# Kernel tuning notes

Hardware: AMD Instinct MI355X
Metric: run time of the kernel (lower is better)

Reference implementation:

```python
import math
import jax, jax.numpy as jnp
import numpy as np

N_HEADS = 16
D_EMBED = 1024
D_HEAD = D_EMBED // N_HEADS
B, S = 4, 2048


def setup_inputs() -> dict:
    key = jax.random.key(0)
    k1, k2, k3, k4, k5 = jax.random.split(key, 5)
    scale_in = 1.0 / math.sqrt(D_EMBED)
    return {
        "x": jax.random.normal(k1, (B, S, D_EMBED), dtype=jnp.float32),
        "w_in": jax.random.normal(k2, (3 * D_EMBED, D_EMBED), dtype=jnp.float32) * scale_in,
        "b_in": jax.random.normal(k3, (3 * D_EMBED,), dtype=jnp.float32) * 0.02,
        "w_out": jax.random.normal(k4, (D_EMBED, D_EMBED), dtype=jnp.float32) * scale_in,
        "b_out": jax.random.normal(k5, (D_EMBED,), dtype=jnp.float32) * 0.02,
        "causal_mask": 1,
    }


def reference(x, w_in, b_in, w_out, b_out, causal_mask):
    Bn, Sn, D = x.shape
    # fused QKV projection (torch Linear: x @ W.T + b)
    qkv = x @ w_in.T + b_in                       # (B, S, 3D)
    q, k, v = jnp.split(qkv, 3, axis=-1)
    def to_heads(t):
        return t.reshape(Bn, Sn, N_HEADS, D_HEAD).transpose(0, 2, 1, 3)  # (B,H,S,dh)
    q, k, v = to_heads(q), to_heads(k), to_heads(v)
    # manual scaled dot-product attention, full (B,H,S,S) scores
    scores = jnp.einsum("bhqd,bhkd->bhqk", q, k)
    if causal_mask:
        tri = jnp.triu(jnp.ones((Sn, Sn), dtype=bool), k=1)
        scores = jnp.where(tri, -jnp.inf, scores)
    scores = scores / math.sqrt(D_HEAD)
    weights = jax.nn.softmax(scores, axis=-1)
    out = jnp.einsum("bhqk,bhkd->bhqd", weights, v)  # (B,H,S,dh)
    out = out.transpose(0, 2, 1, 3).reshape(Bn, Sn, D)
    return out @ w_out.T + b_out
```

## Files before the change

### kernel.cpp

```cpp
#include <hip/hip_runtime.h>

typedef __bf16 bf16x8 __attribute__((ext_vector_type(8)));
typedef float  f32x4  __attribute__((ext_vector_type(4)));
typedef unsigned int uint;

__device__ inline unsigned short f2bf(float f) {
  union { float f; unsigned int u; } v; v.f = f;
  unsigned int u = v.u;
  unsigned int r = u + 0x7FFF + ((u >> 16) & 1);
  return (unsigned short)(r >> 16);
}

__device__ inline uint pack_bf16_rhu(float a, float b) {
  uint ua = __builtin_bit_cast(uint, a) + 0x8000u;
  uint ub = __builtin_bit_cast(uint, b) + 0x8000u;
  return __builtin_amdgcn_perm(ub, ua, 0x07060302u);
}

__device__ inline void load_lds16(const unsigned short* g, unsigned short* l) {
  __builtin_amdgcn_global_load_lds(
      (const __attribute__((address_space(1))) uint*)(g),
      (__attribute__((address_space(3))) uint*)(l), 16, 0, 0);
}

__device__ inline void cvt4(const float* in, unsigned short* out) {
  float4 f = *reinterpret_cast<const float4*>(in);
  ushort4 o;
  o.x = f2bf(f.x); o.y = f2bf(f.y); o.z = f2bf(f.z); o.w = f2bf(f.w);
  *reinterpret_cast<ushort4*>(out) = o;
}

__global__ void cvt_all(const float* __restrict__ x, const float* __restrict__ w_in,
                        const float* __restrict__ w_out,
                        unsigned short* __restrict__ x_bf,
                        unsigned short* __restrict__ w_in_bf,
                        unsigned short* __restrict__ w_out_bf) {
  const int n1 = 8192 * 1024, n2 = 3072 * 1024;
  int i = (blockIdx.x * blockDim.x + threadIdx.x) * 4;
  if (i < n1)            cvt4(x + i, x_bf + i);
  else if (i < n1 + n2)  cvt4(w_in + (i - n1), w_in_bf + (i - n1));
  else                   cvt4(w_out + (i - n1 - n2), w_out_bf + (i - n1 - n2));
}

template<bool OUT_BF16, bool VSPLIT>
__global__ __launch_bounds__(256) void gemm_bt128(
    const unsigned short* __restrict__ A,
    const unsigned short* __restrict__ B,
    const float* __restrict__ bias,
    void* __restrict__ Cout,
    unsigned short* __restrict__ vt,
    int M, int N, int K, int ldc, float scale, int ncut)
{
  __shared__ __attribute__((aligned(16))) unsigned short As[128 * 64];
  __shared__ __attribute__((aligned(16))) unsigned short Bs[128 * 64];

  const int t    = threadIdx.x;
  const int wave = t >> 6, lane = t & 63;
  const int l16  = lane & 15, quad = lane >> 4;
  const int wr = wave >> 1, wc = wave & 1;
  const int m0 = blockIdx.y * 128, n0 = blockIdx.x * 128;
  const int l8 = l16 & 7;

  f32x4 acc[4][4] = {};

  for (int k0 = 0; k0 < K; k0 += 64) {
#pragma unroll
    for (int i = 0; i < 4; ++i) {
      int chunk = i * 256 + t;
      int row = chunk >> 3, cb = chunk & 7;
      int gcb = cb ^ (row & 7);
      load_lds16(A + (size_t)(m0 + row) * K + k0 + gcb * 8, As + chunk * 8);
    }
#pragma unroll
    for (int i = 0; i < 4; ++i) {
      int chunk = i * 256 + t;
      int row = chunk >> 3, cb = chunk & 7;
      int gcb = cb ^ (row & 7);
      load_lds16(B + (size_t)(n0 + row) * K + k0 + gcb * 8, Bs + chunk * 8);
    }
    __syncthreads();
#pragma unroll
    for (int ks = 0; ks < 2; ++ks) {
      bf16x8 af[4], bfr[4];
#pragma unroll
      for (int mt = 0; mt < 4; ++mt)
        af[mt] = *(const bf16x8*)(As + (wr * 64 + mt * 16 + l16) * 64 +
                                  (((ks * 4 + quad) ^ l8) << 3));
#pragma unroll
      for (int nt = 0; nt < 4; ++nt)
        bfr[nt] = *(const bf16x8*)(Bs + (wc * 64 + nt * 16 + l16) * 64 +
                                   (((ks * 4 + quad) ^ l8) << 3));
#pragma unroll
      for (int mt = 0; mt < 4; ++mt)
#pragma unroll
        for (int nt = 0; nt < 4; ++nt)
          acc[mt][nt] = __builtin_amdgcn_mfma_f32_16x16x32_bf16(af[mt], bfr[nt], acc[mt][nt], 0, 0, 0);
    }
    __syncthreads();
  }

#pragma unroll
  for (int nt = 0; nt < 4; ++nt) {
    int col = n0 + wc * 64 + nt * 16 + l16;
    float bv = bias[col];
    float mlt = (col < ncut) ? scale : 1.0f;
#pragma unroll
    for (int mt = 0; mt < 4; ++mt) {
      int row0 = m0 + wr * 64 + mt * 16 + quad * 4;
      float v0 = (acc[mt][nt][0] + bv) * mlt;
      float v1 = (acc[mt][nt][1] + bv) * mlt;
      float v2 = (acc[mt][nt][2] + bv) * mlt;
      float v3 = (acc[mt][nt][3] + bv) * mlt;
      if (VSPLIT && col >= 2048) {
        int d = col - 2048, h = d >> 6, dd = d & 63;
        int bb = row0 >> 11, s = row0 & 2047;
        uint2 w;
        w.x = pack_bf16_rhu(v0, v1);
        w.y = pack_bf16_rhu(v2, v3);
        *(uint2*)(vt + ((size_t)((bb * 16 + h) * 64 + dd) * 2048 + s)) = w;
      } else {
#pragma unroll
        for (int r = 0; r < 4; ++r) {
          float v = (r == 0) ? v0 : (r == 1) ? v1 : (r == 2) ? v2 : v3;
          if (OUT_BF16)
            ((unsigned short*)Cout)[(size_t)(row0 + r) * ldc + col] = f2bf(v);
          else
            ((float*)Cout)[(size_t)(row0 + r) * ldc + col] = v;
        }
      }
    }
  }
}

__global__ __launch_bounds__(256) void attn(
    const unsigned short* __restrict__ qkv2,
    const unsigned short* __restrict__ vt,
    unsigned short* __restrict__ y,
    const int* __restrict__ flag)
{
  __shared__ __attribute__((aligned(16))) unsigned short Qs[64 * 64];
  __shared__ __attribute__((aligned(16))) unsigned short Ks[64 * 64];
  __shared__ __attribute__((aligned(16))) unsigned short VtF[64 * 64];

  const int t    = threadIdx.x;
  const int wave = t >> 6, lane = t & 63;
  const int l16  = lane & 15, quad = lane >> 4;
  const int l8   = l16 & 7;
  const int idx = blockIdx.x;
  const int bh  = idx & 63;
  const int qt  = 31 - (idx >> 6);
  const int b = bh >> 4, h = bh & 15;
  const int causal = flag[0];
  const int q0 = qt * 64;

  const unsigned short* Qg = qkv2 + (size_t)b * 2048 * 2048 + h * 64;
  const unsigned short* Kg = Qg + 1024;
  const unsigned short* Vtg = vt + (size_t)bh * 64 * 2048;

  const int sr = t >> 2, sg = (t & 3) * 2;
  const int slot0 = sr * 64 + (((sg    ) ^ (sr & 7)) << 3);
  const int slot1 = sr * 64 + (((sg + 1) ^ (sr & 7)) << 3);
  const int vb = t & 3;
  const int vslot0 = sr * 64 + ((( vb     ) ^ (sr & 7)) << 3);
  const int vslot1 = sr * 64 + (((vb + 4) ^ (sr & 7)) << 3);
  const unsigned short* vrow = Vtg + (size_t)sr * 2048;

  {
    const unsigned short* src = Qg + (size_t)(q0 + sr) * 2048 + sg * 8;
    *(uint4*)(Qs + slot0) = *(const uint4*)src;
    *(uint4*)(Qs + slot1) = *(const uint4*)(src + 8);
  }
  __syncthreads();
  bf16x8 qf[2];
  qf[0] = *(const bf16x8*)(Qs + (wave * 16 + l16) * 64 + (((0 * 4 + quad) ^ l8) << 3));
  qf[1] = *(const bf16x8*)(Qs + (wave * 16 + l16) * 64 + (((1 * 4 + quad) ^ l8) << 3));
  __syncthreads();
  unsigned short* Ps = Qs;

  f32x4 ot[4] = {};
  float l_lane = 0.f;
  const int q_glob = q0 + wave * 16 + l16;
  const int jmax = causal ? qt : 31;

  uint4 kreg0, kreg1, vreg0, vreg1;
  {
    const unsigned short* src = Kg + (size_t)sr * 2048 + sg * 8;
    kreg0 = *(const uint4*)src;
    kreg1 = *(const uint4*)(src + 8);
    vreg0 = *(const uint4*)(vrow + vb * 8);
    vreg1 = *(const uint4*)(vrow + vb * 8 + 32);
  }

  for (int j = 0; j <= jmax; ++j) {
    *(uint4*)(Ks + slot0)   = kreg0;
    *(uint4*)(Ks + slot1)   = kreg1;
    *(uint4*)(VtF + vslot0) = vreg0;
    *(uint4*)(VtF + vslot1) = vreg1;
    __syncthreads();

    if (j < jmax) {
      const int kvn = (j + 1) * 64;
      const unsigned short* src = Kg + (size_t)(kvn + sr) * 2048 + sg * 8;
      kreg0 = *(const uint4*)src;
      kreg1 = *(const uint4*)(src + 8);
      vreg0 = *(const uint4*)(vrow + kvn + vb * 8);
      vreg1 = *(const uint4*)(vrow + kvn + vb * 8 + 32);
    }

    f32x4 st[4] = {};
#pragma unroll
    for (int ks = 0; ks < 2; ++ks) {
#pragma unroll
      for (int mt = 0; mt < 4; ++mt) {
        bf16x8 kf = *(const bf16x8*)(Ks + (mt * 16 + l16) * 64 + (((ks * 4 + quad) ^ l8) << 3));
        st[mt] = __builtin_amdgcn_mfma_f32_16x16x32_bf16(kf, qf[ks], st[mt], 0, 0, 0);
      }
    }

    const bool diag = (causal != 0) && (j == qt);
    const int kv0 = j * 64;
#pragma unroll
    for (int mt = 0; mt < 4; ++mt) {
      float p[4];
#pragma unroll
      for (int r = 0; r < 4; ++r) {
        float pv = __builtin_amdgcn_exp2f(st[mt][r]);
        if (diag) {
          int kv = kv0 + mt * 16 + quad * 4 + r;
          if (kv > q_glob) pv = 0.f;
        }
        p[r] = pv;
      }
      l_lane += (p[0] + p[1]) + (p[2] + p[3]);
      uint2 w;
      w.x = pack_bf16_rhu(p[0], p[1]);
      w.y = pack_bf16_rhu(p[2], p[3]);
      *(uint2*)(Ps + (wave * 16 + l16) * 64 +
                ((((mt * 2 + (quad >> 1)) ^ l8) << 3) + (quad & 1) * 4)) = w;
    }
    __threadfence_block();

#pragma unroll
    for (int ks = 0; ks < 2; ++ks) {
      bf16x8 pf = *(const bf16x8*)(Ps + (wave * 16 + l16) * 64 + (((ks * 4 + quad) ^ l8) << 3));
#pragma unroll
      for (int mt = 0; mt < 4; ++mt) {
        bf16x8 vf = *(const bf16x8*)(VtF + (mt * 16 + l16) * 64 + (((ks * 4 + quad) ^ l8) << 3));
        ot[mt] = __builtin_amdgcn_mfma_f32_16x16x32_bf16(vf, pf, ot[mt], 0, 0, 0);
      }
    }
    __syncthreads();
  }

  l_lane += __shfl_xor(l_lane, 16);
  l_lane += __shfl_xor(l_lane, 32);
  float inv = 1.f / l_lane;

#pragma unroll
  for (int mt = 0; mt < 4; ++mt) {
    uint2 w;
    w.x = pack_bf16_rhu(ot[mt][0] * inv, ot[mt][1] * inv);
    w.y = pack_bf16_rhu(ot[mt][2] * inv, ot[mt][3] * inv);
    *(uint2*)(Ps + (wave * 16 + l16) * 64 +
              ((((mt * 2 + (quad >> 1)) ^ l8) << 3) + (quad & 1) * 4)) = w;
  }
  __syncthreads();
  {
    size_t base = ((size_t)b * 2048 + q0 + sr) * 1024 + h * 64 + sg * 8;
    *(uint4*)(y + base)     = *(const uint4*)(Ps + slot0);
    *(uint4*)(y + base + 8) = *(const uint4*)(Ps + slot1);
  }
}

extern "C" void kernel_launch(void* const* d_in, const int* in_sizes, int n_in,
                              void* d_out, int out_size, void* d_ws, size_t ws_size,
                              hipStream_t stream) {
  const float* x     = (const float*)d_in[0];
  const float* w_in  = (const float*)d_in[1];
  const float* b_in  = (const float*)d_in[2];
  const float* w_out = (const float*)d_in[3];
  const float* b_out = (const float*)d_in[4];
  const int*   cmask = (const int*)d_in[5];

  char* ws = (char*)d_ws;
  unsigned short* x_bf     = (unsigned short*)(ws);
  unsigned short* w_in_bf  = (unsigned short*)(ws + 16777216);
  unsigned short* w_out_bf = (unsigned short*)(ws + 23068672);
  unsigned short* qkv2_bf  = (unsigned short*)(ws + 25165824);
  unsigned short* vt_bf    = (unsigned short*)(ws + 58720256);
  unsigned short* y_bf     = (unsigned short*)(ws + 75497472);

  const int ntot = (8192 + 3072 + 1024) * 1024;
  cvt_all<<<dim3(ntot / 4 / 256), 256, 0, stream>>>(x, w_in, w_out, x_bf, w_in_bf, w_out_bf);

  gemm_bt128<true, true><<<dim3(24, 64), 256, 0, stream>>>(
      x_bf, w_in_bf, b_in, qkv2_bf, vt_bf, 8192, 3072, 1024, 2048,
      0.18033688011112042f, 1024);

  attn<<<dim3(2048), 256, 0, stream>>>(qkv2_bf, vt_bf, y_bf, cmask);

  gemm_bt128<false, false><<<dim3(8, 64), 256, 0, stream>>>(
      y_bf, w_out_bf, b_out, d_out, nullptr, 8192, 1024, 1024, 1024, 1.0f, 0);
}
```

Measured before the change: 252.4 us.

## Double attention query tile to 128 rows with 512 threads sharing K/V tiles

The attention kernel now processes 128 query rows per block with 8 waves instead of 64 rows with 4 waves, so each K/V tile staged in LDS is reused by twice as many queries and the grid is halved. Waves whose query rows lie entirely before a causal KV tile skip the MFMA and softmax work, and the diagonal mask test becomes per-lane. s_setprio is raised around the MFMA sections. The cost is more waves sitting idle at barriers on the diagonal tiles, plus higher LDS use and a larger block that can lower occupancy.

Measured after the change: 255.9 us. About the same (+1.4%).

```diff
diff --git a/kernel.cpp b/kernel.cpp
--- a/kernel.cpp
+++ b/kernel.cpp
@@ -132,13 +132,13 @@
   }
 }
 
-__global__ __launch_bounds__(256) void attn(
+__global__ __launch_bounds__(512) void attn(
     const unsigned short* __restrict__ qkv2,
     const unsigned short* __restrict__ vt,
     unsigned short* __restrict__ y,
     const int* __restrict__ flag)
 {
-  __shared__ __attribute__((aligned(16))) unsigned short Qs[64 * 64];
+  __shared__ __attribute__((aligned(16))) unsigned short Qs[128 * 64];
   __shared__ __attribute__((aligned(16))) unsigned short Ks[64 * 64];
   __shared__ __attribute__((aligned(16))) unsigned short VtF[64 * 64];
 
@@ -148,10 +148,10 @@
   const int l8   = l16 & 7;
   const int idx = blockIdx.x;
   const int bh  = idx & 63;
-  const int qt  = 31 - (idx >> 6);
+  const int qt  = 15 - (idx >> 6);
   const int b = bh >> 4, h = bh & 15;
   const int causal = flag[0];
-  const int q0 = qt * 64;
+  const int q0 = qt * 128;
 
   const unsigned short* Qg = qkv2 + (size_t)b * 2048 * 2048 + h * 64;
   const unsigned short* Kg = Qg + 1024;
@@ -160,10 +160,8 @@
   const int sr = t >> 2, sg = (t & 3) * 2;
   const int slot0 = sr * 64 + (((sg    ) ^ (sr & 7)) << 3);
   const int slot1 = sr * 64 + (((sg + 1) ^ (sr & 7)) << 3);
-  const int vb = t & 3;
-  const int vslot0 = sr * 64 + ((( vb     ) ^ (sr & 7)) << 3);
-  const int vslot1 = sr * 64 + (((vb + 4) ^ (sr & 7)) << 3);
-  const unsigned short* vrow = Vtg + (size_t)sr * 2048;
+  const int kr = t >> 3, kg = t & 7;
+  const int kslot = kr * 64 + ((kg ^ (kr & 7)) << 3);
 
   {
     const unsigned short* src = Qg + (size_t)(q0 + sr) * 2048 + sg * 8;
@@ -172,82 +170,82 @@
   }
   __syncthreads();
   bf16x8 qf[2];
-  qf[0] = *(const bf16x8*)(Qs + (wave * 16 + l16) * 64 + (((0 * 4 + quad) ^ l8) << 3));
-  qf[1] = *(const bf16x8*)(Qs + (wave * 16 + l16) * 64 + (((1 * 4 + quad) ^ l8) << 3));
+  qf[0] = *(const bf16x8*)(Qs + (wave * 16 + l16) * 64 + (((0 + quad) ^ l8) << 3));
+  qf[1] = *(const bf16x8*)(Qs + (wave * 16 + l16) * 64 + (((4 + quad) ^ l8) << 3));
   __syncthreads();
   unsigned short* Ps = Qs;
 
   f32x4 ot[4] = {};
   float l_lane = 0.f;
   const int q_glob = q0 + wave * 16 + l16;
-  const int jmax = causal ? qt : 31;
-
-  uint4 kreg0, kreg1, vreg0, vreg1;
-  {
-    const unsigned short* src = Kg + (size_t)sr * 2048 + sg * 8;
-    kreg0 = *(const uint4*)src;
-    kreg1 = *(const uint4*)(src + 8);
-    vreg0 = *(const uint4*)(vrow + vb * 8);
-    vreg1 = *(const uint4*)(vrow + vb * 8 + 32);
-  }
+  const int wq_max = q0 + wave * 16 + 15;
+  const int jmax = causal ? 2 * qt + 1 : 31;
+
+  const unsigned short* kptr = Kg + (size_t)kr * 2048 + kg * 8;
+  const unsigned short* vptr = Vtg + (size_t)kr * 2048 + kg * 8;
+  uint4 kreg = *(const uint4*)kptr;
+  uint4 vreg = *(const uint4*)vptr;
 
   for (int j = 0; j <= jmax; ++j) {
-    *(uint4*)(Ks + slot0)   = kreg0;
-    *(uint4*)(Ks + slot1)   = kreg1;
-    *(uint4*)(VtF + vslot0) = vreg0;
-    *(uint4*)(VtF + vslot1) = vreg1;
+    *(uint4*)(Ks + kslot)  = kreg;
+    *(uint4*)(VtF + kslot) = vreg;
     __syncthreads();
 
     if (j < jmax) {
-      const int kvn = (j + 1) * 64;
-      const unsigned short* src = Kg + (size_t)(kvn + sr) * 2048 + sg * 8;
-      kreg0 = *(const uint4*)src;
-      kreg1 = *(const uint4*)(src + 8);
-      vreg0 = *(const uint4*)(vrow + kvn + vb * 8);
-      vreg1 = *(const uint4*)(vrow + kvn + vb * 8 + 32);
-    }
-
-    f32x4 st[4] = {};
-#pragma unroll
-    for (int ks = 0; ks < 2; ++ks) {
+      kptr += 64 * 2048;
+      vptr += 64;
+      kreg = *(const uint4*)kptr;
+      vreg = *(const uint4*)vptr;
+    }
+
+    const bool active = !causal || ((j << 6) <= wq_max);
+    if (active) {
+      f32x4 st[4] = {};
+      __builtin_amdgcn_s_setprio(1);
+#pragma unroll
+      for (int ks = 0; ks < 2; ++ks) {
+#pragma unroll
+        for (int mt = 0; mt < 4; ++mt) {
+          bf16x8 kf = *(const bf16x8*)(Ks + (mt * 16 + l16) * 64 + (((ks * 4 + quad) ^ l8) << 3));
+          st[mt] = __builtin_amdgcn_mfma_f32_16x16x32_bf16(kf, qf[ks], st[mt], 0, 0, 0);
+        }
+      }
+      __builtin_amdgcn_s_setprio(0);
+
+      const int kv0 = j << 6;
+      const bool diag = (causal != 0) && (kv0 + 63 > q_glob);
 #pragma unroll
       for (int mt = 0; mt < 4; ++mt) {
-        bf16x8 kf = *(const bf16x8*)(Ks + (mt * 16 + l16) * 64 + (((ks * 4 + quad) ^ l8) << 3));
-        st[mt] = __builtin_amdgcn_mfma_f32_16x16x32_bf16(kf, qf[ks], st[mt], 0, 0, 0);
+        float p[4];
+#pragma unroll
+        for (int r = 0; r < 4; ++r) {
+          float pv = __builtin_amdgcn_exp2f(st[mt][r]);
+          if (diag) {
+            int kv = kv0 + mt * 16 + quad * 4 + r;
+            if (kv > q_glob) pv = 0.f;
+          }
+          p[r] = pv;
+        }
+        l_lane += (p[0] + p[1]) + (p[2] + p[3]);
+        uint2 w;
+        w.x = pack_bf16_rhu(p[0], p[1]);
+        w.y = pack_bf16_rhu(p[2], p[3]);
+        *(uint2*)(Ps + (wave * 16 + l16) * 64 +
+                  ((((mt * 2 + (quad >> 1)) ^ l8) << 3) + (quad & 1) * 4)) = w;
       }
-    }
-
-    const bool diag = (causal != 0) && (j == qt);
-    const int kv0 = j * 64;
-#pragma unroll
-    for (int mt = 0; mt < 4; ++mt) {
-      float p[4];
-#pragma unroll
-      for (int r = 0; r < 4; ++r) {
-        float pv = __builtin_amdgcn_exp2f(st[mt][r]);
-        if (diag) {
-          int kv = kv0 + mt * 16 + quad * 4 + r;
-          if (kv > q_glob) pv = 0.f;
+      __threadfence_block();
+
+      __builtin_amdgcn_s_setprio(1);
+#pragma unroll
+      for (int ks = 0; ks < 2; ++ks) {
+        bf16x8 pf = *(const bf16x8*)(Ps + (wave * 16 + l16) * 64 + (((ks * 4 + quad) ^ l8) << 3));
+#pragma unroll
+        for (int mt = 0; mt < 4; ++mt) {
+          bf16x8 vf = *(const bf16x8*)(VtF + (mt * 16 + l16) * 64 + (((ks * 4 + quad) ^ l8) << 3));
+          ot[mt] = __builtin_amdgcn_mfma_f32_16x16x32_bf16(vf, pf, ot[mt], 0, 0, 0);
         }
-        p[r] = pv;
       }
-      l_lane += (p[0] + p[1]) + (p[2] + p[3]);
-      uint2 w;
-      w.x = pack_bf16_rhu(p[0], p[1]);
-      w.y = pack_bf16_rhu(p[2], p[3]);
-      *(uint2*)(Ps + (wave * 16 + l16) * 64 +
-                ((((mt * 2 + (quad >> 1)) ^ l8) << 3) + (quad & 1) * 4)) = w;
-    }
-    __threadfence_block();
-
-#pragma unroll
-    for (int ks = 0; ks < 2; ++ks) {
-      bf16x8 pf = *(const bf16x8*)(Ps + (wave * 16 + l16) * 64 + (((ks * 4 + quad) ^ l8) << 3));
-#pragma unroll
-      for (int mt = 0; mt < 4; ++mt) {
-        bf16x8 vf = *(const bf16x8*)(VtF + (mt * 16 + l16) * 64 + (((ks * 4 + quad) ^ l8) << 3));
-        ot[mt] = __builtin_amdgcn_mfma_f32_16x16x32_bf16(vf, pf, ot[mt], 0, 0, 0);
-      }
+      __builtin_amdgcn_s_setprio(0);
     }
     __syncthreads();
   }
@@ -297,7 +295,7 @@
       x_bf, w_in_bf, b_in, qkv2_bf, vt_bf, 8192, 3072, 1024, 2048,
       0.18033688011112042f, 1024);
 
-  attn<<<dim3(2048), 256, 0, stream>>>(qkv2_bf, vt_bf, y_bf, cmask);
+  attn<<<dim3(1024), 512, 0, stream>>>(qkv2_bf, vt_bf, y_bf, cmask);
 
   gemm_bt128<false, false><<<dim3(8, 64), 256, 0, stream>>>(
       y_bf, w_out_bf, b_out, d_out, nullptr, 8192, 1024, 1024, 1024, 1.0f, 0);
```
